# Kernel optimization log

Measured on AMD Instinct MI355X. Metric: run time of the kernel, lower is better.

The kernel has to match this reference:

```python
import jax, jax.numpy as jnp
import numpy as np

HID = 2048      # hidden_size
EXP = 64        # moe_num_experts
TOPK = 2        # moe_top_k
TOL = 1e-4
EPS = 1e-8


def setup_inputs() -> dict:
    key = jax.random.key(0)
    kx, kw = jax.random.split(key)
    x = jax.random.normal(kx, (2048, 8, HID), dtype=jnp.float32)          # (sl, bs, hs)
    W = jax.random.normal(kw, (EXP, HID), dtype=jnp.float32) * 0.02       # router weight (E, H)
    return {"x": x, "W": W}


def sinkhorn(cost, tol=TOL):
    """Iterative Sinkhorn normalization of a (tokens, experts) cost matrix."""
    cost = jnp.exp(cost)
    n0, n1 = cost.shape

    def cond(state):
        _, _, err = state
        return err > tol

    def body(state):
        _, d1_old, _ = state
        d0 = (1.0 / n0) / (jnp.sum(d1_old * cost, axis=1) + EPS)           # (tokens,)
        d1 = (1.0 / n1) / (jnp.sum(d0[:, None] * cost, axis=0) + EPS)      # (experts,)
        err = jnp.mean(jnp.abs(d1_old - d1))
        return (d0, d1, err)

    d0 = jnp.ones((n0,), cost.dtype)
    d1 = jnp.ones((n1,), cost.dtype)
    err0 = jnp.asarray(1e9, cost.dtype)
    d0, d1, _ = jax.lax.while_loop(cond, body, (d0, d1, err0))
    return d1 * cost * d0[:, None]


def reference(x, W):
    # Training-mode path on expert-parallel rank 0 (single device reference).
    tokens = x.reshape(-1, x.shape[-1])                                    # (sl*bs, H)
    logits = tokens @ W.T                                                  # (sl*bs, E)
    # Sinkhorn assignment is computed under no_grad in the original.
    norm_logits = sinkhorn(jax.lax.stop_gradient(logits.astype(jnp.float32)))
    _, indices = jax.lax.top_k(norm_logits, TOPK)                          # (sl*bs, top_k)
    # top_k > 1 -> softmax activation (in fp32, cast back)
    probs = jax.nn.softmax(logits.astype(jnp.float32), axis=-1).astype(logits.dtype)
    scores = jnp.take_along_axis(probs, indices, axis=1)                   # (sl*bs, top_k)
    return scores, indices
```

## Files before the change

kernel.cpp:

```cpp
#include <hip/hip_runtime.h>
#include <hip/hip_cooperative_groups.h>
#include <math.h>

#define HID   2048
#define NEXP  64
#define NTOK  16384
#define SBLK  64
#define TOLF  1e-4f
#define EPSF  1e-8f

template <int KS>
__global__ __launch_bounds__(256) void gemm_logits(const float* __restrict__ x,
                                                   const float* __restrict__ W,
                                                   float* __restrict__ P) {
    __shared__ float xs[64 * 36];
    __shared__ float wTs[32 * 68];

    const int tile = blockIdx.x & 255;
    const int half = blockIdx.x >> 8;
    const int tid  = (int)threadIdx.x;
    const int kb   = half * (HID / KS);
    constexpr int nch = (HID / KS) >> 5;
    const int tb   = tile * 64;

    const int f8 = tid & 7;
    const int r0 = tid >> 3;
    const int tx = tid & 15;
    const int ty = tid >> 4;

    float acc[4][4];
#pragma unroll
    for (int j = 0; j < 4; ++j) {
        acc[j][0] = 0.f; acc[j][1] = 0.f; acc[j][2] = 0.f; acc[j][3] = 0.f;
    }

    const float* xb0 = x + (size_t)(tb + r0) * HID + kb + f8 * 4;
    const float* xb1 = xb0 + (size_t)32 * HID;
    const float* wb0 = W + (size_t)r0 * HID + kb + f8 * 4;
    const float* wb1 = wb0 + (size_t)32 * HID;

    float4 px0, px1, pw0, pw1;
    px0 = *(const float4*)xb0;
    px1 = *(const float4*)xb1;
    pw0 = *(const float4*)wb0;
    pw1 = *(const float4*)wb1;

    for (int c = 0; c < nch; ++c) {
        *(float4*)&xs[r0 * 36 + f8 * 4]        = px0;
        *(float4*)&xs[(r0 + 32) * 36 + f8 * 4] = px1;
        {
            const int ko = 4 * f8;
            wTs[(ko + 0) * 68 + r0] = pw0.x;
            wTs[(ko + 1) * 68 + r0] = pw0.y;
            wTs[(ko + 2) * 68 + r0] = pw0.z;
            wTs[(ko + 3) * 68 + r0] = pw0.w;
            wTs[(ko + 0) * 68 + r0 + 32] = pw1.x;
            wTs[(ko + 1) * 68 + r0 + 32] = pw1.y;
            wTs[(ko + 2) * 68 + r0 + 32] = pw1.z;
            wTs[(ko + 3) * 68 + r0 + 32] = pw1.w;
        }
        __syncthreads();

        if (c + 1 < nch) {
            const int ko = (c + 1) * 32;
            px0 = *(const float4*)(xb0 + ko);
            px1 = *(const float4*)(xb1 + ko);
            pw0 = *(const float4*)(wb0 + ko);
            pw1 = *(const float4*)(wb1 + ko);
        }

#pragma unroll
        for (int kk = 0; kk < 32; kk += 4) {
            const float4 B0 = *(const float4*)&wTs[(kk + 0) * 68 + tx * 4];
            const float4 B1 = *(const float4*)&wTs[(kk + 1) * 68 + tx * 4];
            const float4 B2 = *(const float4*)&wTs[(kk + 2) * 68 + tx * 4];
            const float4 B3 = *(const float4*)&wTs[(kk + 3) * 68 + tx * 4];
#pragma unroll
            for (int j = 0; j < 4; ++j) {
                const float4 A = *(const float4*)&xs[(j * 16 + ty) * 36 + kk];
                acc[j][0] = fmaf(A.x, B0.x, acc[j][0]);
                acc[j][1] = fmaf(A.x, B0.y, acc[j][1]);
                acc[j][2] = fmaf(A.x, B0.z, acc[j][2]);
                acc[j][3] = fmaf(A.x, B0.w, acc[j][3]);
                acc[j][0] = fmaf(A.y, B1.x, acc[j][0]);
                acc[j][1] = fmaf(A.y, B1.y, acc[j][1]);
                acc[j][2] = fmaf(A.y, B1.z, acc[j][2]);
                acc[j][3] = fmaf(A.y, B1.w, acc[j][3]);
                acc[j][0] = fmaf(A.z, B2.x, acc[j][0]);
                acc[j][1] = fmaf(A.z, B2.y, acc[j][1]);
                acc[j][2] = fmaf(A.z, B2.z, acc[j][2]);
                acc[j][3] = fmaf(A.z, B2.w, acc[j][3]);
                acc[j][0] = fmaf(A.w, B3.x, acc[j][0]);
                acc[j][1] = fmaf(A.w, B3.y, acc[j][1]);
                acc[j][2] = fmaf(A.w, B3.z, acc[j][2]);
                acc[j][3] = fmaf(A.w, B3.w, acc[j][3]);
            }
        }
        __syncthreads();
    }

    float* Pb = P + (size_t)half * NTOK * NEXP + (size_t)tb * NEXP;
#pragma unroll
    for (int j = 0; j < 4; ++j) {
        *(float4*)(Pb + (size_t)(j * 16 + ty) * NEXP + tx * 4) =
            make_float4(acc[j][0], acc[j][1], acc[j][2], acc[j][3]);
    }
}

__global__ __launch_bounds__(256) void reduce_halves(const float* __restrict__ P,
                                                     float* __restrict__ L,
                                                     int KS) {
    const size_t i = ((size_t)blockIdx.x * 256 + threadIdx.x) * 4;
    float4 s = *(const float4*)(P + i);
    for (int h = 1; h < KS; ++h) {
        const float4 v = *(const float4*)(P + (size_t)h * NTOK * NEXP + i);
        s.x += v.x; s.y += v.y; s.z += v.z; s.w += v.w;
    }
    *(float4*)(L + i) = s;
}

__global__ __launch_bounds__(1024) void sinkhorn_router(const float* __restrict__ L,
                                                        float* __restrict__ colbuf,
                                                        float* __restrict__ out,
                                                        int nh) {
    cooperative_groups::grid_group grid = cooperative_groups::this_grid();

    __shared__ float part[16][64];
    __shared__ float redq[64][17];
    __shared__ float d1s[64];
    __shared__ float err_s;

    const int b     = blockIdx.x;
    const int tid   = (int)threadIdx.x;
    const int w     = tid >> 6;
    const int lane  = tid & 63;
    const int tbase = b * 256 + w * 16;

    float logit[16], cost[16], dreg[16];
#pragma unroll
    for (int j = 0; j < 16; ++j) {
        const int t = tbase + j;
        float l = L[(size_t)t * NEXP + lane];
        for (int h = 1; h < nh; ++h)
            l += L[(size_t)h * NTOK * NEXP + (size_t)t * NEXP + lane];
        logit[j] = l;
        cost[j]  = expf(l);
        dreg[j]  = 0.0f;
    }

    float d1l   = 1.0f;
    float d1old = 1.0f;
    int   g     = 0;

    for (;;) {
        float colacc = 0.0f;
#pragma unroll
        for (int j = 0; j < 16; ++j) {
            float s = d1l * cost[j];
#pragma unroll
            for (int m = 32; m; m >>= 1) s += __shfl_xor(s, m, 64);
            const float d0 = (1.0f / 16384.0f) / (s + EPSF);
            dreg[j] = d0;
            colacc = fmaf(d0, cost[j], colacc);
        }
        part[w][lane] = colacc;
        __syncthreads();

        float* cb = colbuf + (size_t)(g & 1) * (NEXP * SBLK);
        if (tid < 64) {
            float s = part[0][tid];
#pragma unroll
            for (int q = 1; q < 16; ++q) s += part[q][tid];
            cb[tid * SBLK + b] = s;
        }
        grid.sync();

        {
            const int e = tid >> 4;
            const int q = tid & 15;
            const float4 v = *(const float4*)(cb + e * SBLK + q * 4);
            redq[e][q] = (v.x + v.y) + (v.z + v.w);
        }
        __syncthreads();

        if (tid < 64) {
            float tot = redq[tid][0];
#pragma unroll
            for (int q = 1; q < 16; ++q) tot += redq[tid][q];
            const float d1n = (1.0f / 64.0f) / (tot + EPSF);
            float diff = fabsf(d1old - d1n);
#pragma unroll
            for (int m = 32; m; m >>= 1) diff += __shfl_xor(diff, m, 64);
            d1s[tid] = d1n;
            d1old    = d1n;
            if (tid == 0) err_s = diff * (1.0f / 64.0f);
        }
        __syncthreads();
        d1l = d1s[lane];
        const float err = err_s;
        ++g;
        if (!(err > TOLF) || g >= 512) break;
    }

#pragma unroll 1
    for (int j = 0; j < 16; ++j) {
        const int t = tbase + j;
        const float v = (d1l * cost[j]) * dreg[j];

        float bv = v; int bi = lane;
#pragma unroll
        for (int m = 32; m; m >>= 1) {
            const float ov = __shfl_xor(bv, m, 64);
            const int   oi = __shfl_xor(bi, m, 64);
            if (ov > bv || (ov == bv && oi < bi)) { bv = ov; bi = oi; }
        }
        const int i1 = bi;

        const float v2 = (lane == i1) ? -INFINITY : v;
        float bv2 = v2; int bi2 = lane;
#pragma unroll
        for (int m = 32; m; m >>= 1) {
            const float ov = __shfl_xor(bv2, m, 64);
            const int   oi = __shfl_xor(bi2, m, 64);
            if (ov > bv2 || (ov == bv2 && oi < bi2)) { bv2 = ov; bi2 = oi; }
        }
        const int i2 = bi2;

        float mx = logit[j];
#pragma unroll
        for (int m = 32; m; m >>= 1) mx = fmaxf(mx, __shfl_xor(mx, m, 64));
        const float e = expf(logit[j] - mx);
        float se = e;
#pragma unroll
        for (int m = 32; m; m >>= 1) se += __shfl_xor(se, m, 64);

        const float p1 = __shfl(e, i1, 64) / se;
        const float p2 = __shfl(e, i2, 64) / se;

        if (lane == 0) {
            out[(size_t)t * 2 + 0] = p1;
            out[(size_t)t * 2 + 1] = p2;
            out[(size_t)NTOK * 2 + (size_t)t * 2 + 0] = (float)i1;
            out[(size_t)NTOK * 2 + (size_t)t * 2 + 1] = (float)i2;
        }
    }
}

extern "C" void kernel_launch(void* const* d_in, const int* in_sizes, int n_in,
                              void* d_out, int out_size, void* d_ws, size_t ws_size,
                              hipStream_t stream) {
    const float* x = (const float*)d_in[0];
    const float* W = (const float*)d_in[1];
    float* out = (float*)d_out;

    const size_t PE      = (size_t)NTOK * NEXP;
    const size_t colElts = (size_t)2 * NEXP * SBLK;

    const size_t need8 = (8 * PE + PE + colElts) * sizeof(float);
    const size_t need2 = (2 * PE + PE + colElts) * sizeof(float);

    float* P = (float*)d_ws;
    if (ws_size >= need8) {
        float* L      = P + 8 * PE;
        float* colbuf = L + PE;
        gemm_logits<8><<<dim3(256 * 8), dim3(256), 0, stream>>>(x, W, P);
        reduce_halves<<<dim3(1024), dim3(256), 0, stream>>>(P, L, 8);
        int nh = 1;
        void* args[] = { (void*)&L, (void*)&colbuf, (void*)&out, (void*)&nh };
        hipLaunchCooperativeKernel((void*)sinkhorn_router, dim3(SBLK), dim3(1024),
                                   args, 0, stream);
    } else if (ws_size >= need2) {
        float* L      = P + 2 * PE;
        float* colbuf = L + PE;
        gemm_logits<2><<<dim3(256 * 2), dim3(256), 0, stream>>>(x, W, P);
        reduce_halves<<<dim3(1024), dim3(256), 0, stream>>>(P, L, 2);
        int nh = 1;
        void* args[] = { (void*)&L, (void*)&colbuf, (void*)&out, (void*)&nh };
        hipLaunchCooperativeKernel((void*)sinkhorn_router, dim3(SBLK), dim3(1024),
                                   args, 0, stream);
    } else {
        float* colbuf = P + 2 * PE;
        gemm_logits<2><<<dim3(256 * 2), dim3(256), 0, stream>>>(x, W, P);
        int nh = 2;
        void* args[] = { (void*)&P, (void*)&colbuf, (void*)&out, (void*)&nh };
        hipLaunchCooperativeKernel((void*)sinkhorn_router, dim3(SBLK), dim3(1024),
                                   args, 0, stream);
    }
}
```

Baseline: 302.3 us.

## Replace FP32 SIMT logits GEMM with split-FP16 MFMA GEMM

Replaces the shared-memory FP32 FMA GEMM, its split-K partial buffers and the reduction kernel with a matrix-core GEMM. Each FP32 operand is split into an FP16 high part and a scaled FP16 low part, and three MFMA products (hh, hl, lh) are summed to approximate FP32 accuracy. W is converted once per call by a small kernel, while x is split in registers. This removes the split-K partial writes and the separate reduce pass, in exchange for dropping the low-low term, which may shift logits slightly and change top-k ties near the Sinkhorn tolerance.

```diff
diff --git a/kernel.cpp b/kernel.cpp
--- a/kernel.cpp
+++ b/kernel.cpp
@@ -9,114 +9,102 @@
 #define TOLF  1e-4f
 #define EPSF  1e-8f
 
-template <int KS>
-__global__ __launch_bounds__(256) void gemm_logits(const float* __restrict__ x,
-                                                   const float* __restrict__ W,
-                                                   float* __restrict__ P) {
-    __shared__ float xs[64 * 36];
-    __shared__ float wTs[32 * 68];
-
-    const int tile = blockIdx.x & 255;
-    const int half = blockIdx.x >> 8;
-    const int tid  = (int)threadIdx.x;
-    const int kb   = half * (HID / KS);
-    constexpr int nch = (HID / KS) >> 5;
-    const int tb   = tile * 64;
-
-    const int f8 = tid & 7;
-    const int r0 = tid >> 3;
-    const int tx = tid & 15;
-    const int ty = tid >> 4;
-
-    float acc[4][4];
-#pragma unroll
-    for (int j = 0; j < 4; ++j) {
-        acc[j][0] = 0.f; acc[j][1] = 0.f; acc[j][2] = 0.f; acc[j][3] = 0.f;
-    }
-
-    const float* xb0 = x + (size_t)(tb + r0) * HID + kb + f8 * 4;
-    const float* xb1 = xb0 + (size_t)32 * HID;
-    const float* wb0 = W + (size_t)r0 * HID + kb + f8 * 4;
-    const float* wb1 = wb0 + (size_t)32 * HID;
-
-    float4 px0, px1, pw0, pw1;
-    px0 = *(const float4*)xb0;
-    px1 = *(const float4*)xb1;
-    pw0 = *(const float4*)wb0;
-    pw1 = *(const float4*)wb1;
-
-    for (int c = 0; c < nch; ++c) {
-        *(float4*)&xs[r0 * 36 + f8 * 4]        = px0;
-        *(float4*)&xs[(r0 + 32) * 36 + f8 * 4] = px1;
-        {
-            const int ko = 4 * f8;
-            wTs[(ko + 0) * 68 + r0] = pw0.x;
-            wTs[(ko + 1) * 68 + r0] = pw0.y;
-            wTs[(ko + 2) * 68 + r0] = pw0.z;
-            wTs[(ko + 3) * 68 + r0] = pw0.w;
-            wTs[(ko + 0) * 68 + r0 + 32] = pw1.x;
-            wTs[(ko + 1) * 68 + r0 + 32] = pw1.y;
-            wTs[(ko + 2) * 68 + r0 + 32] = pw1.z;
-            wTs[(ko + 3) * 68 + r0 + 32] = pw1.w;
-        }
-        __syncthreads();
-
-        if (c + 1 < nch) {
-            const int ko = (c + 1) * 32;
-            px0 = *(const float4*)(xb0 + ko);
-            px1 = *(const float4*)(xb1 + ko);
-            pw0 = *(const float4*)(wb0 + ko);
-            pw1 = *(const float4*)(wb1 + ko);
-        }
-
-#pragma unroll
-        for (int kk = 0; kk < 32; kk += 4) {
-            const float4 B0 = *(const float4*)&wTs[(kk + 0) * 68 + tx * 4];
-            const float4 B1 = *(const float4*)&wTs[(kk + 1) * 68 + tx * 4];
-            const float4 B2 = *(const float4*)&wTs[(kk + 2) * 68 + tx * 4];
-            const float4 B3 = *(const float4*)&wTs[(kk + 3) * 68 + tx * 4];
-#pragma unroll
-            for (int j = 0; j < 4; ++j) {
-                const float4 A = *(const float4*)&xs[(j * 16 + ty) * 36 + kk];
-                acc[j][0] = fmaf(A.x, B0.x, acc[j][0]);
-                acc[j][1] = fmaf(A.x, B0.y, acc[j][1]);
-                acc[j][2] = fmaf(A.x, B0.z, acc[j][2]);
-                acc[j][3] = fmaf(A.x, B0.w, acc[j][3]);
-                acc[j][0] = fmaf(A.y, B1.x, acc[j][0]);
-                acc[j][1] = fmaf(A.y, B1.y, acc[j][1]);
-                acc[j][2] = fmaf(A.y, B1.z, acc[j][2]);
-                acc[j][3] = fmaf(A.y, B1.w, acc[j][3]);
-                acc[j][0] = fmaf(A.z, B2.x, acc[j][0]);
-                acc[j][1] = fmaf(A.z, B2.y, acc[j][1]);
-                acc[j][2] = fmaf(A.z, B2.z, acc[j][2]);
-                acc[j][3] = fmaf(A.z, B2.w, acc[j][3]);
-                acc[j][0] = fmaf(A.w, B3.x, acc[j][0]);
-                acc[j][1] = fmaf(A.w, B3.y, acc[j][1]);
-                acc[j][2] = fmaf(A.w, B3.z, acc[j][2]);
-                acc[j][3] = fmaf(A.w, B3.w, acc[j][3]);
-            }
-        }
-        __syncthreads();
-    }
-
-    float* Pb = P + (size_t)half * NTOK * NEXP + (size_t)tb * NEXP;
-#pragma unroll
-    for (int j = 0; j < 4; ++j) {
-        *(float4*)(Pb + (size_t)(j * 16 + ty) * NEXP + tx * 4) =
-            make_float4(acc[j][0], acc[j][1], acc[j][2], acc[j][3]);
-    }
-}
-
-__global__ __launch_bounds__(256) void reduce_halves(const float* __restrict__ P,
-                                                     float* __restrict__ L,
-                                                     int KS) {
-    const size_t i = ((size_t)blockIdx.x * 256 + threadIdx.x) * 4;
-    float4 s = *(const float4*)(P + i);
-    for (int h = 1; h < KS; ++h) {
-        const float4 v = *(const float4*)(P + (size_t)h * NTOK * NEXP + i);
-        s.x += v.x; s.y += v.y; s.z += v.z; s.w += v.w;
-    }
-    *(float4*)(L + i) = s;
+typedef _Float16 f16x8 __attribute__((ext_vector_type(8)));
+typedef float    f32x4 __attribute__((ext_vector_type(4)));
+
+__global__ __launch_bounds__(256) void convert_w(const float* __restrict__ W,
+                                                 _Float16* __restrict__ Wh,
+                                                 _Float16* __restrict__ Wl) {
+    const int i = ((int)blockIdx.x * 256 + (int)threadIdx.x) * 8;
+    const float4 w0 = *(const float4*)(W + i);
+    const float4 w1 = *(const float4*)(W + i + 4);
+    float v[8] = {w0.x, w0.y, w0.z, w0.w, w1.x, w1.y, w1.z, w1.w};
+    f16x8 h, l;
+#pragma unroll
+    for (int j = 0; j < 8; ++j) {
+        const _Float16 hh = (_Float16)v[j];
+        h[j] = hh;
+        l[j] = (_Float16)((v[j] - (float)hh) * 2048.0f);
+    }
+    *(f16x8*)(Wh + i) = h;
+    *(f16x8*)(Wl + i) = l;
+}
+
+__global__ __launch_bounds__(256) void gemm_mfma(const float* __restrict__ x,
+                                                 const _Float16* __restrict__ Wh,
+                                                 const _Float16* __restrict__ Wl,
+                                                 float* __restrict__ L) {
+    const int wave = (int)threadIdx.x >> 6;
+    const int lane = (int)threadIdx.x & 63;
+    const int lo = lane & 15;
+    const int hi = lane >> 4;
+    const int t0 = (int)blockIdx.x * 64 + wave * 16;
+
+    const float*    xp  = x  + (size_t)(t0 + lo) * HID + hi * 8;
+    const _Float16* bhp = Wh + (size_t)lo * HID + hi * 8;
+    const _Float16* blp = Wl + (size_t)lo * HID + hi * 8;
+
+    f32x4 acc_hh[4], acc_hl[4];
+#pragma unroll
+    for (int n = 0; n < 4; ++n) {
+        acc_hh[n] = f32x4{0.f, 0.f, 0.f, 0.f};
+        acc_hl[n] = f32x4{0.f, 0.f, 0.f, 0.f};
+    }
+
+    float4 a0n = *(const float4*)(xp);
+    float4 a1n = *(const float4*)(xp + 4);
+    f16x8 bhn[4], bln[4];
+#pragma unroll
+    for (int n = 0; n < 4; ++n) {
+        bhn[n] = *(const f16x8*)(bhp + n * 16 * HID);
+        bln[n] = *(const f16x8*)(blp + n * 16 * HID);
+    }
+
+#pragma unroll 2
+    for (int s = 0; s < 64; ++s) {
+        const float4 a0 = a0n, a1 = a1n;
+        f16x8 bh[4], bl[4];
+#pragma unroll
+        for (int n = 0; n < 4; ++n) { bh[n] = bhn[n]; bl[n] = bln[n]; }
+
+        const int ko = ((s + 1 < 64) ? (s + 1) : 63) * 32;
+        a0n = *(const float4*)(xp + ko);
+        a1n = *(const float4*)(xp + ko + 4);
+#pragma unroll
+        for (int n = 0; n < 4; ++n) {
+            bhn[n] = *(const f16x8*)(bhp + n * 16 * HID + ko);
+            bln[n] = *(const f16x8*)(blp + n * 16 * HID + ko);
+        }
+
+        f16x8 ah, al;
+        const float av[8] = {a0.x, a0.y, a0.z, a0.w, a1.x, a1.y, a1.z, a1.w};
+#pragma unroll
+        for (int j = 0; j < 8; ++j) {
+            const _Float16 hh = (_Float16)av[j];
+            ah[j] = hh;
+            al[j] = (_Float16)((av[j] - (float)hh) * 2048.0f);
+        }
+
+#pragma unroll
+        for (int n = 0; n < 4; ++n)
+            acc_hh[n] = __builtin_amdgcn_mfma_f32_16x16x32_f16(ah, bh[n], acc_hh[n], 0, 0, 0);
+#pragma unroll
+        for (int n = 0; n < 4; ++n)
+            acc_hl[n] = __builtin_amdgcn_mfma_f32_16x16x32_f16(ah, bl[n], acc_hl[n], 0, 0, 0);
+#pragma unroll
+        for (int n = 0; n < 4; ++n)
+            acc_hl[n] = __builtin_amdgcn_mfma_f32_16x16x32_f16(al, bh[n], acc_hl[n], 0, 0, 0);
+    }
+
+    float* Lb = L + (size_t)(t0 + hi * 4) * NEXP + lo;
+#pragma unroll
+    for (int n = 0; n < 4; ++n) {
+#pragma unroll
+        for (int r = 0; r < 4; ++r) {
+            Lb[(size_t)r * NEXP + n * 16] =
+                acc_hh[n][r] + acc_hl[n][r] * (1.0f / 2048.0f);
+        }
+    }
 }
 
 __global__ __launch_bounds__(1024) void sinkhorn_router(const float* __restrict__ L,
@@ -253,37 +241,16 @@
     const float* W = (const float*)d_in[1];
     float* out = (float*)d_out;
 
-    const size_t PE      = (size_t)NTOK * NEXP;
-    const size_t colElts = (size_t)2 * NEXP * SBLK;
-
-    const size_t need8 = (8 * PE + PE + colElts) * sizeof(float);
-    const size_t need2 = (2 * PE + PE + colElts) * sizeof(float);
-
-    float* P = (float*)d_ws;
-    if (ws_size >= need8) {
-        float* L      = P + 8 * PE;
-        float* colbuf = L + PE;
-        gemm_logits<8><<<dim3(256 * 8), dim3(256), 0, stream>>>(x, W, P);
-        reduce_halves<<<dim3(1024), dim3(256), 0, stream>>>(P, L, 8);
-        int nh = 1;
-        void* args[] = { (void*)&L, (void*)&colbuf, (void*)&out, (void*)&nh };
-        hipLaunchCooperativeKernel((void*)sinkhorn_router, dim3(SBLK), dim3(1024),
-                                   args, 0, stream);
-    } else if (ws_size >= need2) {
-        float* L      = P + 2 * PE;
-        float* colbuf = L + PE;
-        gemm_logits<2><<<dim3(256 * 2), dim3(256), 0, stream>>>(x, W, P);
-        reduce_halves<<<dim3(1024), dim3(256), 0, stream>>>(P, L, 2);
-        int nh = 1;
-        void* args[] = { (void*)&L, (void*)&colbuf, (void*)&out, (void*)&nh };
-        hipLaunchCooperativeKernel((void*)sinkhorn_router, dim3(SBLK), dim3(1024),
-                                   args, 0, stream);
-    } else {
-        float* colbuf = P + 2 * PE;
-        gemm_logits<2><<<dim3(256 * 2), dim3(256), 0, stream>>>(x, W, P);
-        int nh = 2;
-        void* args[] = { (void*)&P, (void*)&colbuf, (void*)&out, (void*)&nh };
-        hipLaunchCooperativeKernel((void*)sinkhorn_router, dim3(SBLK), dim3(1024),
-                                   args, 0, stream);
-    }
-}
+    _Float16* Wh = (_Float16*)d_ws;
+    _Float16* Wl = Wh + (size_t)NEXP * HID;
+    float* L      = (float*)((char*)d_ws + 524288);
+    float* colbuf = L + (size_t)NTOK * NEXP;
+
+    convert_w<<<dim3(64), dim3(256), 0, stream>>>(W, Wh, Wl);
+    gemm_mfma<<<dim3(256), dim3(256), 0, stream>>>(x, Wh, Wl, L);
+
+    int nh = 1;
+    void* args[] = { (void*)&L, (void*)&colbuf, (void*)&out, (void*)&nh };
+    hipLaunchCooperativeKernel((void*)sinkhorn_router, dim3(SBLK), dim3(1024),
+                               args, 0, stream);
+}
```

New measurement: 335.3 us. 10.9% more time.
